# Performance work log

Hardware: AMD Instinct MI355X
Metric: run time of the kernel (lower is better)

Reference implementation:

```python
import jax, jax.numpy as jnp
import numpy as np

IN_DIM = 512
NUM_HEADS = 8
KD = IN_DIM // 2   # 256
VD = IN_DIM        # 512
NEG = -1e9


def setup_inputs() -> dict:
    key = jax.random.key(0)
    k0, k1, k2, k3, k4 = jax.random.split(key, 5)
    B, C, H, W = 2, IN_DIM, 64, 64
    s = lambda fan_in: 1.0 / np.sqrt(fan_in)
    return {
        "X": jax.random.normal(k0, (B, C, H, W), dtype=jnp.float32),
        "Wq": jax.random.normal(k1, (IN_DIM, KD), dtype=jnp.float32) * s(IN_DIM),
        "Wk": jax.random.normal(k2, (IN_DIM, KD), dtype=jnp.float32) * s(IN_DIM),
        "Wv": jax.random.normal(k3, (IN_DIM, VD), dtype=jnp.float32) * s(IN_DIM),
        "Wo": jax.random.normal(k4, (VD, IN_DIM), dtype=jnp.float32) * s(VD),
    }


def reference(X, Wq, Wk, Wv, Wo):
    B, C, H, W = X.shape
    S = H * W
    x = jnp.transpose(X, (0, 2, 3, 1)).reshape(B, S, C)  # [B,S,C]
    dk = KD // NUM_HEADS
    dv = VD // NUM_HEADS
    # projections + head split -> [B,h,S,d]
    q = (x @ Wq).reshape(B, S, NUM_HEADS, dk).transpose(0, 2, 1, 3)
    k = (x @ Wk).reshape(B, S, NUM_HEADS, dk).transpose(0, 2, 1, 3)
    v = (x @ Wv).reshape(B, S, NUM_HEADS, dv).transpose(0, 2, 1, 3)
    q = q * (dk ** -0.5)
    logits = jnp.einsum('bhqd,bhkd->bhqk', q, k)
    bias = NEG * jnp.triu(jnp.ones((S, S), dtype=logits.dtype), 1)  # causal
    weights = jax.nn.softmax(logits + bias, axis=-1)
    out = weights @ v                                  # [B,h,S,dv]
    out = out.transpose(0, 2, 1, 3).reshape(B, S, VD)  # merge heads
    out = out @ Wo
    return out.reshape(B, H, W, C)
```

## Files before the change

### kernel.cpp

```cpp
#include <hip/hip_runtime.h>
#include <hip/hip_bf16.h>
#include <math.h>

#define BATCH 2
#define CH 512
#define SEQ 4096
#define KDIM 256
#define VDIM 512
#define NHEADS 8
#define DK 32
#define DV 64

typedef unsigned short u16;
typedef unsigned int u32;
typedef __attribute__((ext_vector_type(8))) short bf16x8;
typedef __attribute__((ext_vector_type(4))) float f32x4;

__device__ __forceinline__ u16 f2bf(float f) {
    u32 x = __float_as_uint(f);
    u32 r = (x + 0x7fffu + ((x >> 16) & 1u)) >> 16;
    return (u16)r;
}
__device__ __forceinline__ u16 f2bf_fast(float f) {
    return (u16)((__float_as_uint(f) + 0x8000u) >> 16);
}
__device__ __forceinline__ u32 pack2f(float lo, float hi) {
    return (u32)f2bf_fast(lo) | (((__float_as_uint(hi) + 0x8000u) >> 16) << 16);
}
__device__ __forceinline__ u32 cvtpk_bf16(float lo, float hi) {
    u32 r;
    asm("v_cvt_pk_bf16_f32 %0, %1, %2" : "=v"(r) : "v"(lo), "v"(hi));
    return r;
}

#define QSCALE (0.17677669529663687f * 1.4426950408889634f)


__global__ __launch_bounds__(256) void prep(
    const float* __restrict__ X,
    const float* __restrict__ Wq, const float* __restrict__ Wk,
    const float* __restrict__ Wv, const float* __restrict__ Wo,
    u16* __restrict__ Xb16, u16* __restrict__ Wall, u16* __restrict__ WoT)
{
    __shared__ u16 T[64 * 72];
    const int bid = blockIdx.x;
    const int t = threadIdx.x;
    const int tr = t >> 4;
    const int tc4 = (t & 15) * 4;

    const float* src; u16* dst;
    int src_row0, src_col0, src_pitch, dst_row0, dst_col0, dst_pitch;
    float scale = 1.0f;

    if (bid < 1024) {
        const int b = bid >> 9, rem = bid & 511;
        const int st = rem >> 3, ct = rem & 7;
        src = X + (size_t)b * CH * SEQ;
        src_row0 = ct * 64; src_col0 = st * 64; src_pitch = SEQ;
        dst = Xb16 + (size_t)b * SEQ * CH;
        dst_row0 = st * 64; dst_col0 = ct * 64; dst_pitch = CH;
    } else if (bid < 1152) {
        const int r = bid - 1024;
        const int nt = r >> 3, ct = r & 7;
        if (nt < 4)      { src = Wq; src_col0 = nt * 64;       src_pitch = KDIM; scale = QSCALE; }
        else if (nt < 8) { src = Wk; src_col0 = (nt - 4) * 64; src_pitch = KDIM; }
        else             { src = Wv; src_col0 = (nt - 8) * 64; src_pitch = VDIM; }
        src_row0 = ct * 64;
        dst = Wall; dst_row0 = nt * 64; dst_col0 = ct * 64; dst_pitch = 512;
    } else {
        const int r = bid - 1152;
        const int kt = r >> 3, nt = r & 7;
        src = Wo; src_row0 = kt * 64; src_col0 = nt * 64; src_pitch = 512;
        dst = WoT; dst_row0 = nt * 64; dst_col0 = kt * 64; dst_pitch = 512;
    }

#pragma unroll
    for (int j = 0; j < 4; ++j) {
        const int row = j * 16 + tr;
        const float4 v = *reinterpret_cast<const float4*>(
            &src[(size_t)(src_row0 + row) * src_pitch + src_col0 + tc4]);
        T[(tc4 + 0) * 72 + row] = f2bf(v.x * scale);
        T[(tc4 + 1) * 72 + row] = f2bf(v.y * scale);
        T[(tc4 + 2) * 72 + row] = f2bf(v.z * scale);
        T[(tc4 + 3) * 72 + row] = f2bf(v.w * scale);
    }
    __syncthreads();
#pragma unroll
    for (int j = 0; j < 4; ++j) {
        const int orow = j * 16 + tr;
        const ushort4 o = *reinterpret_cast<ushort4*>(&T[orow * 72 + tc4]);
        *reinterpret_cast<ushort4*>(
            &dst[(size_t)(dst_row0 + orow) * dst_pitch + dst_col0 + tc4]) = o;
    }
}

__global__ __launch_bounds__(256, 2) void qkv3(
    const u16* __restrict__ Xb16, const u16* __restrict__ Wall,
    u16* __restrict__ Qh, u16* __restrict__ Kh, u16* __restrict__ Vh)
{
    __shared__ __align__(16) u16 As[2][128 * 40];
    __shared__ __align__(16) u16 Bs[2][128 * 40];
    const int tid = threadIdx.x;
    const int wv = tid >> 6, lane = tid & 63;
    const int c = lane & 15, quad = lane >> 4;
    const int wm = wv & 1, wn = wv >> 1;
    const int m0 = blockIdx.x * 128;
    const int ny = blockIdx.y;
    const int n0 = ny * 128;

    u16* Y; int N, nbase;
    if (ny < 2)      { Y = Qh; N = KDIM; nbase = 0; }
    else if (ny < 4) { Y = Kh; N = KDIM; nbase = 256; }
    else             { Y = Vh; N = VDIM; nbase = 512; }

    const int srow = tid >> 1, scol = (tid & 1) * 16;

    f32x4 acc[4][4];
#pragma unroll
    for (int i = 0; i < 4; ++i)
#pragma unroll
        for (int g = 0; g < 4; ++g) acc[i][g] = (f32x4){0.f, 0.f, 0.f, 0.f};

    uint4 ar0, ar1, br0, br1;
    auto ld = [&](int k0) {
        const uint4* ap = reinterpret_cast<const uint4*>(
            &Xb16[(size_t)(m0 + srow) * 512 + k0 + scol]);
        ar0 = ap[0]; ar1 = ap[1];
        const uint4* bp = reinterpret_cast<const uint4*>(
            &Wall[(size_t)(n0 + srow) * 512 + k0 + scol]);
        br0 = bp[0]; br1 = bp[1];
    };
    auto stage = [&](int buf) {
        uint4* ad = reinterpret_cast<uint4*>(&As[buf][srow * 40 + scol]);
        ad[0] = ar0; ad[1] = ar1;
        uint4* bd = reinterpret_cast<uint4*>(&Bs[buf][srow * 40 + scol]);
        bd[0] = br0; bd[1] = br1;
    };

    ld(0);
    stage(0);
    ld(32);

    for (int i = 0; i < 16; ++i) {
        const int cur = i & 1;
        __syncthreads();
        stage(cur ^ 1);
        const int k0n = (i + 2 < 16) ? (i + 2) * 32 : 15 * 32;
        ld(k0n);
        bf16x8 af[4], bf_[4];
#pragma unroll
        for (int j = 0; j < 4; ++j) {
            af[j] = *reinterpret_cast<bf16x8*>(
                &As[cur][(wm * 64 + 16 * j + c) * 40 + quad * 8]);
            bf_[j] = *reinterpret_cast<bf16x8*>(
                &Bs[cur][(wn * 64 + 16 * j + c) * 40 + quad * 8]);
        }
#pragma unroll
        for (int j = 0; j < 4; ++j)
#pragma unroll
            for (int g = 0; g < 4; ++g)
                acc[j][g] = __builtin_amdgcn_mfma_f32_16x16x32_bf16(
                    af[j], bf_[g], acc[j][g], 0, 0, 0);
    }
#pragma unroll
    for (int j = 0; j < 4; ++j)
#pragma unroll
        for (int r = 0; r < 4; ++r) {
            const int row = m0 + wm * 64 + 16 * j + quad * 4 + r;
            const int col = n0 - nbase + wn * 64 + c;
#pragma unroll
            for (int g = 0; g < 4; ++g)
                Y[(size_t)row * N + col + 16 * g] = f2bf(acc[j][g][r]);
        }
}

__global__ __launch_bounds__(256, 2) void oproj3(
    const u16* __restrict__ A, const u16* __restrict__ WoT,
    float* __restrict__ Out)
{
    __shared__ __align__(16) u16 As[2][128 * 40];
    __shared__ __align__(16) u16 Bs[2][64 * 40];
    const int tid = threadIdx.x;
    const int wv = tid >> 6, lane = tid & 63;
    const int c = lane & 15, quad = lane >> 4;
    const int wm = wv & 1, wn = wv >> 1;
    const int m0 = blockIdx.x * 128;
    const int n0 = blockIdx.y * 64;

    const int srow = tid >> 1, scol = (tid & 1) * 16;
    const int srB = tid >> 2, scB = (tid & 3) * 8;

    f32x4 acc[4][2];
#pragma unroll
    for (int j = 0; j < 4; ++j)
#pragma unroll
        for (int g = 0; g < 2; ++g) acc[j][g] = (f32x4){0.f, 0.f, 0.f, 0.f};

    uint4 ar0, ar1, br0;
    auto ld = [&](int k0) {
        const uint4* ap = reinterpret_cast<const uint4*>(
            &A[(size_t)(m0 + srow) * 512 + k0 + scol]);
        ar0 = ap[0]; ar1 = ap[1];
        br0 = *reinterpret_cast<const uint4*>(
            &WoT[(size_t)(n0 + srB) * 512 + k0 + scB]);
    };
    auto stage = [&](int buf) {
        uint4* ad = reinterpret_cast<uint4*>(&As[buf][srow * 40 + scol]);
        ad[0] = ar0; ad[1] = ar1;
        *reinterpret_cast<uint4*>(&Bs[buf][srB * 40 + scB]) = br0;
    };

    ld(0);
    stage(0);
    ld(32);

    for (int i = 0; i < 16; ++i) {
        const int cur = i & 1;
        __syncthreads();
        stage(cur ^ 1);
        const int k0n = (i + 2 < 16) ? (i + 2) * 32 : 15 * 32;
        ld(k0n);
        bf16x8 af[4], bf_[2];
#pragma unroll
        for (int j = 0; j < 4; ++j)
            af[j] = *reinterpret_cast<bf16x8*>(
                &As[cur][(wm * 64 + 16 * j + c) * 40 + quad * 8]);
#pragma unroll
        for (int g = 0; g < 2; ++g)
            bf_[g] = *reinterpret_cast<bf16x8*>(
                &Bs[cur][(wn * 32 + 16 * g + c) * 40 + quad * 8]);
#pragma unroll
        for (int j = 0; j < 4; ++j)
#pragma unroll
            for (int g = 0; g < 2; ++g)
                acc[j][g] = __builtin_amdgcn_mfma_f32_16x16x32_bf16(
                    af[j], bf_[g], acc[j][g], 0, 0, 0);
    }
#pragma unroll
    for (int j = 0; j < 4; ++j)
#pragma unroll
        for (int r = 0; r < 4; ++r) {
            const int row = m0 + wm * 64 + 16 * j + quad * 4 + r;
            const int col = n0 + wn * 32 + c;
#pragma unroll
            for (int g = 0; g < 2; ++g)
                Out[(size_t)row * 512 + col + 16 * g] = acc[j][g][r];
        }
}

#define KSW(row, col) ((row) * 32 + ((col) ^ (((row) & 3) << 3)))
#define VSW(row, col) ((row) * 64 + ((col) ^ (((row) & 7) << 3)))

__global__ __launch_bounds__(512, 4) void flash_mfma(
    const u16* __restrict__ Q, const u16* __restrict__ K,
    const u16* __restrict__ V, u16* __restrict__ AO)
{
    __shared__ __align__(16) union {
        struct {
            u16 Kl[2][2][64 * 32];
            u16 Vt[2][2][64 * 64];
        } t;
        float mg[4][64][40];
    } sh;

    const int tid  = threadIdx.x;
    const int w    = tid >> 6;
    const int ws   = w & 3;
    const int wg   = w >> 2;
    const int lane = tid & 63;
    const int c    = lane & 15;
    const int quad = lane >> 4;
    const int h = blockIdx.y, b = blockIdx.z;

    const int qbA = blockIdx.x;
    const int qbB = 63 - qbA;
    const int q0A = qbA * 64, q0B = qbB * 64;

    const u16* Qb = Q + (size_t)b * SEQ * KDIM + h * DK;
    const u16* Kb = K + (size_t)b * SEQ * KDIM + h * DK;
    const u16* Vb = V + (size_t)b * SEQ * VDIM + h * DV;
    u16* AOb = AO + (size_t)b * SEQ * VDIM + h * DV;

    const bf16x8 qfA = *reinterpret_cast<const bf16x8*>(
        &Qb[(size_t)(q0A + ws * 16 + c) * KDIM + quad * 8]);
    const bf16x8 qfB = *reinterpret_cast<const bf16x8*>(
        &Qb[(size_t)(q0B + ws * 16 + c) * KDIM + quad * 8]);

    const bf16x8 ones = {(short)0x3F80, (short)0x3F80, (short)0x3F80, (short)0x3F80,
                         (short)0x3F80, (short)0x3F80, (short)0x3F80, (short)0x3F80};

    f32x4 oA[4], oB[4];
#pragma unroll
    for (int g = 0; g < 4; ++g) {
        oA[g] = (f32x4){0.f, 0.f, 0.f, 0.f};
        oB[g] = (f32x4){0.f, 0.f, 0.f, 0.f};
    }
    f32x4 laccA = {0.f, 0.f, 0.f, 0.f}, laccB = {0.f, 0.f, 0.f, 0.f};

    const int t256 = tid & 255;
    const int krow = t256 >> 2, kc8 = (t256 & 3) * 8;
    const int vs0 = (t256 & 31) * 2, vd0 = (t256 >> 5) * 8;

    const int qrbase = ws * 16 + c;
    const int T = (qbB >> 1) + 1;

    uint4 kreg, vra, vrb;
    auto ldtile = [&](int kb) {
        const int k0 = kb * 64;
        kreg = *reinterpret_cast<const uint4*>(&Kb[(size_t)(k0 + krow) * KDIM + kc8]);
        vra  = *reinterpret_cast<const uint4*>(&Vb[(size_t)(k0 + vs0) * VDIM + vd0]);
        vrb  = *reinterpret_cast<const uint4*>(&Vb[(size_t)(k0 + vs0 + 1) * VDIM + vd0]);
    };
    auto stagetile = [&](int buf) {
        *reinterpret_cast<uint4*>(&sh.t.Kl[wg][buf][KSW(krow, kc8)]) = kreg;
        union { uint4 q; u16 s[8]; } ra, rb;
        ra.q = vra; rb.q = vrb;
#pragma unroll
        for (int i = 0; i < 8; ++i) {
            u32 packed = (u32)ra.s[i] | ((u32)rb.s[i] << 16);
            *reinterpret_cast<u32*>(&sh.t.Vt[wg][buf][VSW(vd0 + i, vs0)]) = packed;
        }
    };

    ldtile(wg);
    stagetile(0);
    ldtile(2 + wg);

    for (int it = 0; it < T; ++it) {
        const int kb = 2 * it + wg;
        const int k0 = kb * 64;
        const int cur = it & 1;
        __syncthreads();
        stagetile(cur ^ 1);
        {
            int kbn = 2 * (it + 2) + wg; if (kbn > 63) kbn = 63;
            ldtile(kbn);
        }
        const u16* Klc = sh.t.Kl[wg][cur];
        const u16* Vtc = sh.t.Vt[wg][cur];

        auto compute = [&](const bf16x8& qf, int q0, bool diag,
                           f32x4* o, f32x4& lacc) {
            f32x4 s[4];
#pragma unroll
            for (int g = 0; g < 4; ++g) {
                const bf16x8 kf = *reinterpret_cast<const bf16x8*>(
                    &Klc[KSW(c + 16 * g, quad * 8)]);
                const f32x4 z = {0.f, 0.f, 0.f, 0.f};
                s[g] = __builtin_amdgcn_mfma_f32_16x16x32_bf16(kf, qf, z, 0, 0, 0);
            }
            if (diag) {
                const int qr = q0 + qrbase;
#pragma unroll
                for (int g = 0; g < 4; ++g) {
                    const int kc0 = k0 + 16 * g + quad * 4;
#pragma unroll
                    for (int r = 0; r < 4; ++r)
                        if (kc0 + r > qr) s[g][r] = -1e30f;
                }
            }
            u32 wk[4][2];
#pragma unroll
            for (int g = 0; g < 4; ++g)
#pragma unroll
                for (int j2 = 0; j2 < 2; ++j2)
                    wk[g][j2] = cvtpk_bf16(
                        __builtin_amdgcn_exp2f(s[g][2 * j2]),
                        __builtin_amdgcn_exp2f(s[g][2 * j2 + 1]));
            union { u32 wq[4]; bf16x8 v; } ub0, ub1;
#pragma unroll
            for (int j2 = 0; j2 < 2; ++j2) {
                {
                    auto t1 = __builtin_amdgcn_permlane32_swap(
                        wk[0][j2], wk[1][j2], false, false);
                    auto t2 = __builtin_amdgcn_permlane16_swap(
                        (u32)t1[0], (u32)t1[1], false, false);
                    ub0.wq[j2]     = (u32)t2[0];
                    ub0.wq[2 + j2] = (u32)t2[1];
                }
                {
                    auto t1 = __builtin_amdgcn_permlane32_swap(
                        wk[2][j2], wk[3][j2], false, false);
                    auto t2 = __builtin_amdgcn_permlane16_swap(
                        (u32)t1[0], (u32)t1[1], false, false);
                    ub1.wq[j2]     = (u32)t2[0];
                    ub1.wq[2 + j2] = (u32)t2[1];
                }
            }
            const bf16x8 pb0 = ub0.v, pb1 = ub1.v;
            lacc = __builtin_amdgcn_mfma_f32_16x16x32_bf16(ones, pb0, lacc, 0, 0, 0);
            lacc = __builtin_amdgcn_mfma_f32_16x16x32_bf16(ones, pb1, lacc, 0, 0, 0);
#pragma unroll
            for (int g = 0; g < 4; ++g) {
                const bf16x8 v0 = *reinterpret_cast<const bf16x8*>(
                    &Vtc[VSW(c + 16 * g, quad * 8)]);
                const bf16x8 v1 = *reinterpret_cast<const bf16x8*>(
                    &Vtc[VSW(c + 16 * g, 32 + quad * 8)]);
                o[g] = __builtin_amdgcn_mfma_f32_16x16x32_bf16(v0, pb0, o[g], 0, 0, 0);
                o[g] = __builtin_amdgcn_mfma_f32_16x16x32_bf16(v1, pb1, o[g], 0, 0, 0);
            }
        };

        if (kb <= qbA) compute(qfA, q0A, kb == qbA, oA, laccA);
        if (kb <= qbB) compute(qfB, q0B, kb == qbB, oB, laccB);
    }

    __syncthreads();
    if (wg == 1) {
        float* m = sh.mg[ws][lane];
#pragma unroll
        for (int g = 0; g < 4; ++g)
#pragma unroll
            for (int r = 0; r < 4; ++r) {
                m[g * 4 + r]      = oA[g][r];
                m[16 + g * 4 + r] = oB[g][r];
            }
        m[32] = laccA[0];
        m[33] = laccB[0];
    }
    __syncthreads();
    if (wg == 0) {
        const float* m = sh.mg[ws][lane];
#pragma unroll
        for (int g = 0; g < 4; ++g)
#pragma unroll
            for (int r = 0; r < 4; ++r) {
                oA[g][r] += m[g * 4 + r];
                oB[g][r] += m[16 + g * 4 + r];
            }
        const float invA = 1.f / (laccA[0] + m[32]);
        const float invB = 1.f / (laccB[0] + m[33]);
        const int rowA = q0A + qrbase;
        const int rowB = q0B + qrbase;
#pragma unroll
        for (int g = 0; g < 4; ++g) {
            ushort4 a4, b4;
            a4.x = f2bf(oA[g][0] * invA); a4.y = f2bf(oA[g][1] * invA);
            a4.z = f2bf(oA[g][2] * invA); a4.w = f2bf(oA[g][3] * invA);
            b4.x = f2bf(oB[g][0] * invB); b4.y = f2bf(oB[g][1] * invB);
            b4.z = f2bf(oB[g][2] * invB); b4.w = f2bf(oB[g][3] * invB);
            *reinterpret_cast<ushort4*>(
                &AOb[(size_t)rowA * VDIM + 16 * g + quad * 4]) = a4;
            *reinterpret_cast<ushort4*>(
                &AOb[(size_t)rowB * VDIM + 16 * g + quad * 4]) = b4;
        }
    }
}

__global__ __launch_bounds__(256) void qkv_proj(
    const float* __restrict__ X,
    const float* __restrict__ Wq, const float* __restrict__ Wk,
    const float* __restrict__ Wv,
    u16* __restrict__ Qh, u16* __restrict__ Kh, u16* __restrict__ Vh)
{
    __shared__ __align__(16) u16 Xs[2][64 * 40];
    __shared__ __align__(16) u16 Wsm[2][64 * 40];
    const int tid = threadIdx.x;
    const int w = tid >> 6, lane = tid & 63;
    const int c = lane & 15, quad = lane >> 4;
    const int s0 = blockIdx.x * 64, b = blockIdx.z;
    const int ny = blockIdx.y;

    const float* Wt; u16* Y; int N, n0; float scale;
    if (ny < 4)       { Wt = Wq; Y = Qh; N = KDIM; n0 = ny * 64;       scale = QSCALE; }
    else if (ny < 8)  { Wt = Wk; Y = Kh; N = KDIM; n0 = (ny - 4) * 64; scale = 1.0f; }
    else              { Wt = Wv; Y = Vh; N = VDIM; n0 = (ny - 8) * 64; scale = 1.0f; }

    const float* Xb = X + (size_t)b * CH * SEQ;
    const int cp = tid >> 4;
    const int s4 = (tid & 15) * 4;

    f32x4 acc[4];
#pragma unroll
    for (int g = 0; g < 4; ++g) acc[g] = (f32x4){0.f, 0.f, 0.f, 0.f};

    auto ldx = [&](int c0, float4& a, float4& bb) {
        a  = *reinterpret_cast<const float4*>(&Xb[(size_t)(c0 + 2 * cp) * SEQ + s0 + s4]);
        bb = *reinterpret_cast<const float4*>(&Xb[(size_t)(c0 + 2 * cp + 1) * SEQ + s0 + s4]);
    };
    auto ldwf = [&](int c0, float4& a, float4& bb) {
        a  = *reinterpret_cast<const float4*>(&Wt[(size_t)(c0 + 2 * cp) * N + n0 + s4]);
        bb = *reinterpret_cast<const float4*>(&Wt[(size_t)(c0 + 2 * cp + 1) * N + n0 + s4]);
    };
    auto stage = [&](int buf, const float4& xa, const float4& xb,
                     const float4& wa, const float4& wb) {
        const float a[4] = {xa.x, xa.y, xa.z, xa.w};
        const float bb[4] = {xb.x, xb.y, xb.z, xb.w};
        const float aw[4] = {wa.x, wa.y, wa.z, wa.w};
        const float bw[4] = {wb.x, wb.y, wb.z, wb.w};
#pragma unroll
        for (int i = 0; i < 4; ++i) {
            *reinterpret_cast<u32*>(&Xs[buf][(s4 + i) * 40 + 2 * cp]) = pack2f(a[i], bb[i]);
            *reinterpret_cast<u32*>(&Wsm[buf][(s4 + i) * 40 + 2 * cp]) = pack2f(aw[i], bw[i]);
        }
    };

    float4 xa, xb, wa, wb;
    ldx(0, xa, xb); ldwf(0, wa, wb);
    stage(0, xa, xb, wa, wb);
    ldx(32, xa, xb); ldwf(32, wa, wb);

    for (int i = 0; i < 16; ++i) {
        const int cur = i & 1;
        __syncthreads();
        stage(cur ^ 1, xa, xb, wa, wb);
        const int c0n = (i + 2 < 16) ? (i + 2) * 32 : 15 * 32;
        ldx(c0n, xa, xb); ldwf(c0n, wa, wb);
        const bf16x8 af = *reinterpret_cast<bf16x8*>(&Xs[cur][(w * 16 + c) * 40 + quad * 8]);
#pragma unroll
        for (int g = 0; g < 4; ++g) {
            bf16x8 bf_ = *reinterpret_cast<bf16x8*>(&Wsm[cur][(c + 16 * g) * 40 + quad * 8]);
            acc[g] = __builtin_amdgcn_mfma_f32_16x16x32_bf16(af, bf_, acc[g], 0, 0, 0);
        }
    }
    u16* Yb = Y + (size_t)b * SEQ * N;
#pragma unroll
    for (int r = 0; r < 4; ++r) {
        const int row = s0 + w * 16 + quad * 4 + r;
#pragma unroll
        for (int g = 0; g < 4; ++g)
            Yb[(size_t)row * N + n0 + c + 16 * g] = f2bf(acc[g][r] * scale);
    }
}

__global__ __launch_bounds__(256) void oproj_mfma(
    const u16* __restrict__ A, const float* __restrict__ Wo,
    float* __restrict__ Out)
{
    __shared__ __align__(16) u16 Ws[2][64 * 40];
    const int tid = threadIdx.x;
    const int w = tid >> 6, lane = tid & 63;
    const int c = lane & 15, quad = lane >> 4;
    const int m0 = blockIdx.x * 64, n0 = blockIdx.y * 64;
    const int kp = tid >> 4;
    const int n4 = (tid & 15) * 4;
    const u16* Arow = &A[(size_t)(m0 + w * 16 + c) * 512];

    f32x4 acc[4];
#pragma unroll
    for (int g = 0; g < 4; ++g) acc[g] = (f32x4){0.f, 0.f, 0.f, 0.f};

    auto ldwf = [&](int k0, float4& a, float4& bb) {
        a  = *reinterpret_cast<const float4*>(&Wo[(size_t)(k0 + 2 * kp) * 512 + n0 + n4]);
        bb = *reinterpret_cast<const float4*>(&Wo[(size_t)(k0 + 2 * kp + 1) * 512 + n0 + n4]);
    };
    auto stage = [&](int buf, const float4& wa, const float4& wb) {
        const float a[4] = {wa.x, wa.y, wa.z, wa.w};
        const float bb[4] = {wb.x, wb.y, wb.z, wb.w};
#pragma unroll
        for (int i = 0; i < 4; ++i)
            *reinterpret_cast<u32*>(&Ws[buf][(n4 + i) * 40 + 2 * kp]) = pack2f(a[i], bb[i]);
    };

    float4 wa, wb;
    ldwf(0, wa, wb);
    stage(0, wa, wb);
    ldwf(32, wa, wb);
    bf16x8 afc = *reinterpret_cast<const bf16x8*>(&Arow[quad * 8]);

    for (int i = 0; i < 16; ++i) {
        const int cur = i & 1;
        __syncthreads();
        stage(cur ^ 1, wa, wb);
        const int k0n = (i + 2 < 16) ? (i + 2) * 32 : 15 * 32;
        ldwf(k0n, wa, wb);
        const int k0a = (i + 1 < 16) ? (i + 1) * 32 : 15 * 32;
        const bf16x8 afn = *reinterpret_cast<const bf16x8*>(&Arow[k0a + quad * 8]);
#pragma unroll
        for (int g = 0; g < 4; ++g) {
            bf16x8 bf_ = *reinterpret_cast<bf16x8*>(&Ws[cur][(c + 16 * g) * 40 + quad * 8]);
            acc[g] = __builtin_amdgcn_mfma_f32_16x16x32_bf16(afc, bf_, acc[g], 0, 0, 0);
        }
        afc = afn;
    }
#pragma unroll
    for (int r = 0; r < 4; ++r) {
        const int row = m0 + w * 16 + quad * 4 + r;
#pragma unroll
        for (int g = 0; g < 4; ++g)
            Out[(size_t)row * 512 + n0 + c + 16 * g] = acc[g][r];
    }
}

extern "C" void kernel_launch(void* const* d_in, const int* in_sizes, int n_in,
                              void* d_out, int out_size, void* d_ws, size_t ws_size,
                              hipStream_t stream) {
    const float* X  = (const float*)d_in[0];
    const float* Wq = (const float*)d_in[1];
    const float* Wk = (const float*)d_in[2];
    const float* Wv = (const float*)d_in[3];
    const float* Wo = (const float*)d_in[4];
    float* out = (float*)d_out;

    const size_t qk = (size_t)BATCH * SEQ * KDIM;
    const size_t vs = (size_t)BATCH * SEQ * VDIM;
    u16* Qh  = (u16*)d_ws;
    u16* Kh  = Qh + qk;
    u16* Vh  = Kh + qk;
    u16* XA  = Vh + vs;
    u16* Wall = XA + vs;
    u16* WoT  = Wall + 1024 * 512;
    const size_t need_fast = (size_t)(WoT + 512 * 512 - (u16*)d_ws) * sizeof(u16);

    if (ws_size >= need_fast) {
        prep<<<dim3(1216), 256, 0, stream>>>(X, Wq, Wk, Wv, Wo, XA, Wall, WoT);
        qkv3<<<dim3((BATCH * SEQ) / 128, 8), 256, 0, stream>>>(XA, Wall, Qh, Kh, Vh);
        flash_mfma<<<dim3(32, NHEADS, BATCH), 512, 0, stream>>>(Qh, Kh, Vh, XA);
        oproj3<<<dim3((BATCH * SEQ) / 128, 8), 256, 0, stream>>>(XA, WoT, out);
    } else {
        u16* AOh = XA;
        qkv_proj<<<dim3(SEQ / 64, 16, BATCH), 256, 0, stream>>>(
            X, Wq, Wk, Wv, Qh, Kh, Vh);
        flash_mfma<<<dim3(32, NHEADS, BATCH), 512, 0, stream>>>(Qh, Kh, Vh, AOh);
        oproj_mfma<<<dim3((BATCH * SEQ) / 64, VDIM / 64), 256, 0, stream>>>(AOh, Wo, out);
    }
}
```

Baseline: 153.7 us.

## Fuse X transpose and bf16 conversion into QKV projection GEMM loader

The prep kernel no longer transposes and converts X into a bf16 staging buffer. Instead the QKV GEMM reads fp32 X directly in channel-major layout, packs channel pairs to bf16 and writes them transposed into a swizzled shared-memory tile. This removes a full write and read of an 8 MB intermediate and most of the prep blocks. In exchange, each of the 8 column-tile blocks now rereads fp32 X (twice the bytes of bf16) and does the conversion redundantly, with more scattered LDS stores.

After: 151.7 us (median of 2 runs). Within noise of the previous version (-1.3%).

```diff
diff --git a/kernel.cpp b/kernel.cpp
--- a/kernel.cpp
+++ b/kernel.cpp
@@ -37,10 +37,9 @@
 
 
 __global__ __launch_bounds__(256) void prep(
-    const float* __restrict__ X,
     const float* __restrict__ Wq, const float* __restrict__ Wk,
     const float* __restrict__ Wv, const float* __restrict__ Wo,
-    u16* __restrict__ Xb16, u16* __restrict__ Wall, u16* __restrict__ WoT)
+    u16* __restrict__ Wall, u16* __restrict__ WoT)
 {
     __shared__ u16 T[64 * 72];
     const int bid = blockIdx.x;
@@ -52,23 +51,15 @@
     int src_row0, src_col0, src_pitch, dst_row0, dst_col0, dst_pitch;
     float scale = 1.0f;
 
-    if (bid < 1024) {
-        const int b = bid >> 9, rem = bid & 511;
-        const int st = rem >> 3, ct = rem & 7;
-        src = X + (size_t)b * CH * SEQ;
-        src_row0 = ct * 64; src_col0 = st * 64; src_pitch = SEQ;
-        dst = Xb16 + (size_t)b * SEQ * CH;
-        dst_row0 = st * 64; dst_col0 = ct * 64; dst_pitch = CH;
-    } else if (bid < 1152) {
-        const int r = bid - 1024;
-        const int nt = r >> 3, ct = r & 7;
+    if (bid < 128) {
+        const int nt = bid >> 3, ct = bid & 7;
         if (nt < 4)      { src = Wq; src_col0 = nt * 64;       src_pitch = KDIM; scale = QSCALE; }
         else if (nt < 8) { src = Wk; src_col0 = (nt - 4) * 64; src_pitch = KDIM; }
         else             { src = Wv; src_col0 = (nt - 8) * 64; src_pitch = VDIM; }
         src_row0 = ct * 64;
         dst = Wall; dst_row0 = nt * 64; dst_col0 = ct * 64; dst_pitch = 512;
     } else {
-        const int r = bid - 1152;
+        const int r = bid - 128;
         const int kt = r >> 3, nt = r & 7;
         src = Wo; src_row0 = kt * 64; src_col0 = nt * 64; src_pitch = 512;
         dst = WoT; dst_row0 = nt * 64; dst_col0 = kt * 64; dst_pitch = 512;
@@ -94,8 +85,10 @@
     }
 }
 
-__global__ __launch_bounds__(256, 2) void qkv3(
-    const u16* __restrict__ Xb16, const u16* __restrict__ Wall,
+#define ASW(row, colu16) ((row) * 40 + ((colu16) ^ ((((row) >> 2) & 3) << 3)))
+
+__global__ __launch_bounds__(256, 2) void qkvX(
+    const float* __restrict__ X, const u16* __restrict__ Wall,
     u16* __restrict__ Qh, u16* __restrict__ Kh, u16* __restrict__ Vh)
 {
     __shared__ __align__(16) u16 As[2][128 * 40];
@@ -113,6 +106,11 @@
     else if (ny < 4) { Y = Kh; N = KDIM; nbase = 256; }
     else             { Y = Vh; N = VDIM; nbase = 512; }
 
+    const int cp = tid >> 4;
+    const int s4 = (tid & 15) * 4;
+    const int bb = m0 >> 12;
+    const float* Xb = X + (size_t)bb * CH * SEQ + (m0 & 4095);
+
     const int srow = tid >> 1, scol = (tid & 1) * 16;
 
     f32x4 acc[4][4];
@@ -121,18 +119,31 @@
 #pragma unroll
         for (int g = 0; g < 4; ++g) acc[i][g] = (f32x4){0.f, 0.f, 0.f, 0.f};
 
-    uint4 ar0, ar1, br0, br1;
+    float4 xa0, xb0, xa1, xb1;
+    uint4 br0, br1;
     auto ld = [&](int k0) {
-        const uint4* ap = reinterpret_cast<const uint4*>(
-            &Xb16[(size_t)(m0 + srow) * 512 + k0 + scol]);
-        ar0 = ap[0]; ar1 = ap[1];
+        const size_t ch0 = (size_t)(k0 + 2 * cp) * SEQ;
+        const size_t ch1 = (size_t)(k0 + 2 * cp + 1) * SEQ;
+        xa0 = *reinterpret_cast<const float4*>(&Xb[ch0 + s4]);
+        xb0 = *reinterpret_cast<const float4*>(&Xb[ch1 + s4]);
+        xa1 = *reinterpret_cast<const float4*>(&Xb[ch0 + 64 + s4]);
+        xb1 = *reinterpret_cast<const float4*>(&Xb[ch1 + 64 + s4]);
         const uint4* bp = reinterpret_cast<const uint4*>(
             &Wall[(size_t)(n0 + srow) * 512 + k0 + scol]);
         br0 = bp[0]; br1 = bp[1];
     };
     auto stage = [&](int buf) {
-        uint4* ad = reinterpret_cast<uint4*>(&As[buf][srow * 40 + scol]);
-        ad[0] = ar0; ad[1] = ar1;
+        const float a0[4] = {xa0.x, xa0.y, xa0.z, xa0.w};
+        const float b0[4] = {xb0.x, xb0.y, xb0.z, xb0.w};
+        const float a1[4] = {xa1.x, xa1.y, xa1.z, xa1.w};
+        const float b1[4] = {xb1.x, xb1.y, xb1.z, xb1.w};
+#pragma unroll
+        for (int i = 0; i < 4; ++i) {
+            *reinterpret_cast<u32*>(&As[buf][ASW(s4 + i, 2 * cp)]) =
+                pack2f(a0[i], b0[i]);
+            *reinterpret_cast<u32*>(&As[buf][ASW(64 + s4 + i, 2 * cp)]) =
+                pack2f(a1[i], b1[i]);
+        }
         uint4* bd = reinterpret_cast<uint4*>(&Bs[buf][srow * 40 + scol]);
         bd[0] = br0; bd[1] = br1;
     };
@@ -151,7 +162,7 @@
 #pragma unroll
         for (int j = 0; j < 4; ++j) {
             af[j] = *reinterpret_cast<bf16x8*>(
-                &As[cur][(wm * 64 + 16 * j + c) * 40 + quad * 8]);
+                &As[cur][ASW(wm * 64 + 16 * j + c, quad * 8)]);
             bf_[j] = *reinterpret_cast<bf16x8*>(
                 &Bs[cur][(wn * 64 + 16 * j + c) * 40 + quad * 8]);
         }
@@ -603,8 +614,8 @@
     const size_t need_fast = (size_t)(WoT + 512 * 512 - (u16*)d_ws) * sizeof(u16);
 
     if (ws_size >= need_fast) {
-        prep<<<dim3(1216), 256, 0, stream>>>(X, Wq, Wk, Wv, Wo, XA, Wall, WoT);
-        qkv3<<<dim3((BATCH * SEQ) / 128, 8), 256, 0, stream>>>(XA, Wall, Qh, Kh, Vh);
+        prep<<<dim3(192), 256, 0, stream>>>(Wq, Wk, Wv, Wo, Wall, WoT);
+        qkvX<<<dim3((BATCH * SEQ) / 128, 8), 256, 0, stream>>>(X, Wall, Qh, Kh, Vh);
         flash_mfma<<<dim3(32, NHEADS, BATCH), 512, 0, stream>>>(Qh, Kh, Vh, XA);
         oproj3<<<dim3((BATCH * SEQ) / 128, 8), 256, 0, stream>>>(XA, WoT, out);
     } else {
```
